# Kernel optimization log

Hardware: AMD Instinct MI355X
Metric: run time of the kernel (lower is better)

The kernel has to match this reference:

```python
import jax, jax.numpy as jnp
import numpy as np

EPS = 1e-8
THRESHOLD_FACTOR = 0.5


def setup_inputs() -> dict:
    key = jax.random.key(0)
    k1, k2, k3 = jax.random.split(key, 3)
    B, S, D_IN, D_OUT = 4, 4096, 2048, 2048
    x = jax.random.normal(k1, (B, S, D_IN), dtype=jnp.float32)
    # kaiming-uniform-like init for weight
    bound = 1.0 / np.sqrt(D_IN)
    weight = jax.random.uniform(k2, (D_OUT, D_IN), dtype=jnp.float32,
                                minval=-np.sqrt(3.0) * bound, maxval=np.sqrt(3.0) * bound)
    row_scale = jnp.ones((D_OUT, 1), dtype=jnp.float32)
    bias = jax.random.uniform(k3, (D_OUT,), dtype=jnp.float32, minval=-bound, maxval=bound)
    g = jnp.ones((D_IN,), dtype=jnp.float32)  # input RMSNorm affine weight
    return {"x": x, "weight": weight, "row_scale": row_scale, "bias": bias, "g": g}


def _rms_norm(v, axis):
    return v * jax.lax.rsqrt(jnp.mean(v * v, axis=axis, keepdims=True) + EPS)


def reference(x, weight, row_scale, bias, g):
    # input RMSNorm with affine scale
    xn = _rms_norm(x, -1) * g  # [B,S,Din]
    # row RMSNorm of weight
    w = _rms_norm(weight, 1)  # [Dout,Din]
    # abs-mean threshold ternary quantization
    abs_mean = jnp.mean(jnp.abs(w), axis=1, keepdims=True)  # [Dout,1]
    mask = (jnp.abs(w) > THRESHOLD_FACTOR * abs_mean).astype(w.dtype)
    w_q = jnp.sign(w) * mask  # ternary {-1,0,1}
    # scaled dequant: per-row abs_mean and learned row_scale
    w_eff = w_q * abs_mean * row_scale  # [Dout,Din]
    out = jnp.einsum('bsd,od->bso', xn, w_eff) + bias
    return out
```

## Files before the change

kernel.cpp:

```cpp
#include <hip/hip_runtime.h>
#include <stdint.h>

#define EPSF 1e-8f

using i32x4 = __attribute__((ext_vector_type(4))) int;

__device__ __forceinline__ float wave_sum(float v) {
#pragma unroll
  for (int off = 32; off > 0; off >>= 1) v += __shfl_down(v, off, 64);
  return v;
}
__device__ __forceinline__ float wave_max(float v) {
#pragma unroll
  for (int off = 32; off > 0; off >>= 1) v = fmaxf(v, __shfl_down(v, off, 64));
  return v;
}

__global__ __launch_bounds__(256) void wquant_kernel(
    const float* __restrict__ w, const float* __restrict__ row_scale,
    signed char* __restrict__ wq, float* __restrict__ scale, int K) {
  const int row = blockIdx.x;
  const int t = threadIdx.x;
  const float* wr = w + (size_t)row * K;
  float4 v0 = reinterpret_cast<const float4*>(wr)[2 * t];
  float4 v1 = reinterpret_cast<const float4*>(wr)[2 * t + 1];
  float f[8] = {v0.x, v0.y, v0.z, v0.w, v1.x, v1.y, v1.z, v1.w};
  float sa = 0.f, sq = 0.f;
#pragma unroll
  for (int i = 0; i < 8; ++i) { sa += fabsf(f[i]); sq += f[i] * f[i]; }
  sa = wave_sum(sa);
  sq = wave_sum(sq);
  __shared__ float smA[4], smQ[4];
  const int wid = t >> 6;
  if ((t & 63) == 0) { smA[wid] = sa; smQ[wid] = sq; }
  __syncthreads();
  const float sumabs = smA[0] + smA[1] + smA[2] + smA[3];
  const float sumsq  = smQ[0] + smQ[1] + smQ[2] + smQ[3];
  const float absmean = sumabs / (float)K;
  const float thr = 0.5f * absmean;
  union { signed char c[8]; uint2 u; } pk;
#pragma unroll
  for (int i = 0; i < 8; ++i)
    pk.c[i] = (fabsf(f[i]) > thr) ? (f[i] > 0.f ? (signed char)1 : (signed char)-1)
                                  : (signed char)0;
  reinterpret_cast<uint2*>(wq + (size_t)row * K)[t] = pk.u;
  if (t == 0)
    scale[row] = absmean * rsqrtf(sumsq / (float)K + EPSF) * row_scale[row];
}

__global__ __launch_bounds__(256) void xnorm_kernel(
    const float* __restrict__ x, const float* __restrict__ g,
    signed char* __restrict__ xq, float* __restrict__ sx, int K) {
  const int row = blockIdx.x;
  const int t = threadIdx.x;
  const float* xr = x + (size_t)row * K;
  float4 v0 = reinterpret_cast<const float4*>(xr)[2 * t];
  float4 v1 = reinterpret_cast<const float4*>(xr)[2 * t + 1];
  float f[8] = {v0.x, v0.y, v0.z, v0.w, v1.x, v1.y, v1.z, v1.w};
  float sq = 0.f;
#pragma unroll
  for (int i = 0; i < 8; ++i) sq += f[i] * f[i];
  sq = wave_sum(sq);
  __shared__ float smQ[4], smM[4];
  const int wid = t >> 6;
  if ((t & 63) == 0) smQ[wid] = sq;
  __syncthreads();
  const float sumsq = smQ[0] + smQ[1] + smQ[2] + smQ[3];
  const float rs = rsqrtf(sumsq / (float)K + EPSF);
  float4 g0 = reinterpret_cast<const float4*>(g)[2 * t];
  float4 g1 = reinterpret_cast<const float4*>(g)[2 * t + 1];
  float gg[8] = {g0.x, g0.y, g0.z, g0.w, g1.x, g1.y, g1.z, g1.w};
  float vv[8]; float am = 0.f;
#pragma unroll
  for (int i = 0; i < 8; ++i) {
    vv[i] = f[i] * rs * gg[i];
    am = fmaxf(am, fabsf(vv[i]));
  }
  am = wave_max(am);
  if ((t & 63) == 0) smM[wid] = am;
  __syncthreads();
  const float amax = fmaxf(fmaxf(smM[0], smM[1]), fmaxf(smM[2], smM[3]));
  const float inv = amax > 0.f ? 127.f / amax : 0.f;
  union { signed char c[8]; uint2 u; } pk;
#pragma unroll
  for (int i = 0; i < 8; ++i)
    pk.c[i] = (signed char)__float2int_rn(vv[i] * inv);
  reinterpret_cast<uint2*>(xq + (size_t)row * K)[t] = pk.u;
  if (t == 0) sx[row] = amax > 0.f ? amax / 127.f : 0.f;
}


#define BAR() do { __builtin_amdgcn_sched_barrier(0); \
                   asm volatile("" ::: "memory"); \
                   __builtin_amdgcn_s_barrier(); \
                   asm volatile("" ::: "memory"); \
                   __builtin_amdgcn_sched_barrier(0); } while (0)
#define VM(n) asm volatile("s_waitcnt vmcnt(" #n ")" ::: "memory")

__global__ __launch_bounds__(512, 2) void gemm_kernel(
    const signed char* __restrict__ A,
    const signed char* __restrict__ B,
    const float* __restrict__ scale, const float* __restrict__ bias,
    const float* __restrict__ sx,
    float* __restrict__ C, int M, int N, int K) {
  __shared__ signed char lds[2][2][2][16384];

  const int tid  = threadIdx.x;
  const int lane = tid & 63;
  const int wid  = tid >> 6;
  const int wm   = wid >> 2;
  const int wn   = wid & 3;
  const int fr   = lane & 15;
  const int kq   = lane >> 4;

  const int nwg = gridDim.x;
  const int cpx = nwg >> 3;
  const int swz = (blockIdx.x & 7) * cpx + (blockIdx.x >> 3);
  const int NBN = N >> 8;
  const int bn = swz % NBN;
  const int bm = swz / NBN;
  const int mBase = bm * 256, nBase = bn * 256;

  const size_t Kb = (size_t)K;

  const int sr = tid >> 3;
  const int gsrc = (tid & 7) ^ (sr & 7);
  const char* Abyte = (const char*)A + (size_t)(mBase + sr) * Kb + gsrc * 16;
  const char* Bbyte = (const char*)B +
      (size_t)(nBase + ((sr >> 5) * 64) + (sr & 31)) * Kb + gsrc * 16;

#define STAGE_A(bufi, h, t) do { \
    __builtin_amdgcn_global_load_lds( \
      (const __attribute__((address_space(1))) void*)(Abyte + (size_t)((h) * 64) * Kb + (size_t)(t) * 128), \
      (__attribute__((address_space(3))) void*)(&lds[bufi][0][h][tid * 16]), 16, 0, 0); \
    __builtin_amdgcn_global_load_lds( \
      (const __attribute__((address_space(1))) void*)(Abyte + (size_t)(128 + (h) * 64) * Kb + (size_t)(t) * 128), \
      (__attribute__((address_space(3))) void*)(&lds[bufi][0][h][8192 + tid * 16]), 16, 0, 0); \
  } while (0)

#define STAGE_B(bufi, h, t) do { \
    __builtin_amdgcn_global_load_lds( \
      (const __attribute__((address_space(1))) void*)(Bbyte + (size_t)((h) * 32) * Kb + (size_t)(t) * 128), \
      (__attribute__((address_space(3))) void*)(&lds[bufi][1][h][tid * 16]), 16, 0, 0); \
    __builtin_amdgcn_global_load_lds( \
      (const __attribute__((address_space(1))) void*)(Bbyte + (size_t)(128 + (h) * 32) * Kb + (size_t)(t) * 128), \
      (__attribute__((address_space(3))) void*)(&lds[bufi][1][h][8192 + tid * 16]), 16, 0, 0); \
  } while (0)

  const int slot0 = ((kq ^ (fr & 7)) << 4);
  const int aRowB = (wm * 64 + fr) * 128;
  const int bRowB = (wn * 32 + fr) * 128;

  i32x4 aF[4][2], bF[4][2];
  i32x4 acc[8][4];
#pragma unroll
  for (int m = 0; m < 8; ++m)
#pragma unroll
    for (int n = 0; n < 4; ++n) acc[m][n] = (i32x4){0, 0, 0, 0};

#define LDA(bufi, mg) do { \
    _Pragma("unroll") for (int mm = 0; mm < 4; ++mm) \
    _Pragma("unroll") for (int s = 0; s < 2; ++s) \
      aF[mm][s] = *(const i32x4*)&lds[bufi][0][mg][ \
          aRowB + mm * 2048 + (slot0 ^ (s << 6))]; \
  } while (0)

#define LDB(bufi, np) do { \
    _Pragma("unroll") for (int nn = 0; nn < 2; ++nn) \
    _Pragma("unroll") for (int s = 0; s < 2; ++s) \
      bF[(np) * 2 + nn][s] = *(const i32x4*)&lds[bufi][1][np][ \
          bRowB + nn * 2048 + (slot0 ^ (s << 6))]; \
  } while (0)

#define MFMA_Q(mg, np) do { \
    __builtin_amdgcn_s_setprio(1); \
    _Pragma("unroll") for (int mm = 0; mm < 4; ++mm) \
    _Pragma("unroll") for (int nn = 0; nn < 2; ++nn) { \
      i32x4 c = acc[(mg) * 4 + mm][(np) * 2 + nn]; \
      c = __builtin_amdgcn_mfma_i32_16x16x64_i8(aF[mm][0], bF[(np) * 2 + nn][0], c, 0, 0, 0); \
      c = __builtin_amdgcn_mfma_i32_16x16x64_i8(aF[mm][1], bF[(np) * 2 + nn][1], c, 0, 0, 0); \
      acc[(mg) * 4 + mm][(np) * 2 + nn] = c; \
    } \
    __builtin_amdgcn_s_setprio(0); } while (0)

  const int crowBase = mBase + wm * 128 + kq * 4;
  const int ccolBase = nBase + wn * 64 + fr;

#define STORE_Q(mg, np) do { \
    float sxq_[4][4]; \
    _Pragma("unroll") for (int mm = 0; mm < 4; ++mm) \
    _Pragma("unroll") for (int r = 0; r < 4; ++r) \
      sxq_[mm][r] = sx[crowBase + ((mg) * 4 + mm) * 16 + r]; \
    _Pragma("unroll") for (int nn = 0; nn < 2; ++nn) { \
      const int gc = ccolBase + ((np) * 2 + nn) * 16; \
      const float sc = scale[gc]; \
      const float bi = bias[gc]; \
      _Pragma("unroll") for (int mm = 0; mm < 4; ++mm) { \
        const int r0 = crowBase + ((mg) * 4 + mm) * 16; \
        _Pragma("unroll") for (int r = 0; r < 4; ++r) \
          C[(size_t)(r0 + r) * (size_t)N + (size_t)gc] = \
              (float)acc[(mg) * 4 + mm][(np) * 2 + nn][r] * (sxq_[mm][r] * sc) + bi; \
      } } } while (0)

  STAGE_A(0, 0, 0); STAGE_B(0, 0, 0);
  STAGE_A(0, 1, 0); STAGE_B(0, 1, 0);
  STAGE_A(1, 0, 1); STAGE_B(1, 0, 1);

  const int NT = K >> 7;
  for (int i = 0; i < (NT >> 1) - 1; ++i) {
    const int t1  = 2 * i + 1;
    const int tn0 = 2 * i + 2;
    const int tn1 = 2 * i + 3;
    VM(4); BAR();
    STAGE_A(1, 1, t1); STAGE_B(1, 1, t1);
    LDA(0, 0); LDB(0, 0); LDB(0, 1);
    MFMA_Q(0, 0); MFMA_Q(0, 1);
    BAR();
    STAGE_A(0, 0, tn0); STAGE_B(0, 0, tn0);
    LDA(0, 1);
    MFMA_Q(1, 0); MFMA_Q(1, 1);
    VM(4); BAR();
    STAGE_A(0, 1, tn0); STAGE_B(0, 1, tn0);
    LDA(1, 0); LDB(1, 0); LDB(1, 1);
    MFMA_Q(0, 0); MFMA_Q(0, 1);
    BAR();
    STAGE_A(1, 0, tn1); STAGE_B(1, 0, tn1);
    LDA(1, 1);
    MFMA_Q(1, 0); MFMA_Q(1, 1);
  }

  {
    const int tl = NT - 1;
    VM(4); BAR();
    STAGE_A(1, 1, tl); STAGE_B(1, 1, tl);
    LDA(0, 0); LDB(0, 0); LDB(0, 1);
    MFMA_Q(0, 0); MFMA_Q(0, 1);
    BAR();
    LDA(0, 1);
    MFMA_Q(1, 0); MFMA_Q(1, 1);
    VM(0); BAR();
    LDA(1, 0); LDB(1, 0); LDB(1, 1);
    MFMA_Q(0, 0); STORE_Q(0, 0);
    MFMA_Q(0, 1); STORE_Q(0, 1);
    BAR();
    LDA(1, 1);
    MFMA_Q(1, 0); STORE_Q(1, 0);
    MFMA_Q(1, 1); STORE_Q(1, 1);
  }
#undef STAGE_A
#undef STAGE_B
#undef LDA
#undef LDB
#undef MFMA_Q
#undef STORE_Q
}

extern "C" void kernel_launch(void* const* d_in, const int* in_sizes, int n_in,
                              void* d_out, int out_size, void* d_ws, size_t ws_size,
                              hipStream_t stream) {
  const float* x         = (const float*)d_in[0];
  const float* weight    = (const float*)d_in[1];
  const float* row_scale = (const float*)d_in[2];
  const float* bias      = (const float*)d_in[3];
  const float* g         = (const float*)d_in[4];
  float* out = (float*)d_out;

  const int Din  = in_sizes[4];
  const int Dout = in_sizes[3];
  const int Mrows = in_sizes[0] / Din;

  char* ws = (char*)d_ws;
  signed char* wq = (signed char*)ws;
  signed char* xq = (signed char*)(ws + (size_t)Dout * Din);
  float* scale = (float*)(ws + (size_t)Dout * Din + (size_t)Mrows * Din);
  float* sx = scale + Dout;

  wquant_kernel<<<Dout, 256, 0, stream>>>(weight, row_scale, wq, scale, Din);
  xnorm_kernel<<<Mrows, 256, 0, stream>>>(x, g, xq, sx, Din);
  const int grid = (Mrows / 256) * (Dout / 256);
  gemm_kernel<<<grid, 512, 0, stream>>>(xq, wq, scale, bias, sx, out,
                                        Mrows, Dout, Din);
}
```

Baseline: 116.4 us.

## Load B fragments directly from global to registers and merge prep kernels

The GEMM stops staging the weight (B) tile through LDS and instead loads each wave's B fragments straight from global memory into registers, double-buffered across two register banks. The A-only LDS buffer is halved and the schedule is rewritten with new vmcnt waits. The two quantization kernels are also merged into one launch to save a kernel launch. The risks are uncoalesced or redundant global B reads across waves, since the four waves sharing a column no longer share an LDS copy, and fragile hand-counted vmcnt values.

```diff
diff --git a/kernel.cpp b/kernel.cpp
--- a/kernel.cpp
+++ b/kernel.cpp
@@ -16,77 +16,76 @@
   return v;
 }
 
-__global__ __launch_bounds__(256) void wquant_kernel(
+__global__ __launch_bounds__(256) void prep_kernel(
+    const float* __restrict__ x, const float* __restrict__ g,
     const float* __restrict__ w, const float* __restrict__ row_scale,
-    signed char* __restrict__ wq, float* __restrict__ scale, int K) {
-  const int row = blockIdx.x;
+    signed char* __restrict__ xq, float* __restrict__ sx,
+    signed char* __restrict__ wq, float* __restrict__ scale,
+    int K, int Dout) {
+  __shared__ float smA[4], smQ[4], smM[4];
   const int t = threadIdx.x;
-  const float* wr = w + (size_t)row * K;
-  float4 v0 = reinterpret_cast<const float4*>(wr)[2 * t];
-  float4 v1 = reinterpret_cast<const float4*>(wr)[2 * t + 1];
-  float f[8] = {v0.x, v0.y, v0.z, v0.w, v1.x, v1.y, v1.z, v1.w};
-  float sa = 0.f, sq = 0.f;
-#pragma unroll
-  for (int i = 0; i < 8; ++i) { sa += fabsf(f[i]); sq += f[i] * f[i]; }
-  sa = wave_sum(sa);
-  sq = wave_sum(sq);
-  __shared__ float smA[4], smQ[4];
   const int wid = t >> 6;
-  if ((t & 63) == 0) { smA[wid] = sa; smQ[wid] = sq; }
-  __syncthreads();
-  const float sumabs = smA[0] + smA[1] + smA[2] + smA[3];
-  const float sumsq  = smQ[0] + smQ[1] + smQ[2] + smQ[3];
-  const float absmean = sumabs / (float)K;
-  const float thr = 0.5f * absmean;
-  union { signed char c[8]; uint2 u; } pk;
-#pragma unroll
-  for (int i = 0; i < 8; ++i)
-    pk.c[i] = (fabsf(f[i]) > thr) ? (f[i] > 0.f ? (signed char)1 : (signed char)-1)
-                                  : (signed char)0;
-  reinterpret_cast<uint2*>(wq + (size_t)row * K)[t] = pk.u;
-  if (t == 0)
-    scale[row] = absmean * rsqrtf(sumsq / (float)K + EPSF) * row_scale[row];
-}
-
-__global__ __launch_bounds__(256) void xnorm_kernel(
-    const float* __restrict__ x, const float* __restrict__ g,
-    signed char* __restrict__ xq, float* __restrict__ sx, int K) {
-  const int row = blockIdx.x;
-  const int t = threadIdx.x;
-  const float* xr = x + (size_t)row * K;
-  float4 v0 = reinterpret_cast<const float4*>(xr)[2 * t];
-  float4 v1 = reinterpret_cast<const float4*>(xr)[2 * t + 1];
-  float f[8] = {v0.x, v0.y, v0.z, v0.w, v1.x, v1.y, v1.z, v1.w};
-  float sq = 0.f;
-#pragma unroll
-  for (int i = 0; i < 8; ++i) sq += f[i] * f[i];
-  sq = wave_sum(sq);
-  __shared__ float smQ[4], smM[4];
-  const int wid = t >> 6;
-  if ((t & 63) == 0) smQ[wid] = sq;
-  __syncthreads();
-  const float sumsq = smQ[0] + smQ[1] + smQ[2] + smQ[3];
-  const float rs = rsqrtf(sumsq / (float)K + EPSF);
-  float4 g0 = reinterpret_cast<const float4*>(g)[2 * t];
-  float4 g1 = reinterpret_cast<const float4*>(g)[2 * t + 1];
-  float gg[8] = {g0.x, g0.y, g0.z, g0.w, g1.x, g1.y, g1.z, g1.w};
-  float vv[8]; float am = 0.f;
-#pragma unroll
-  for (int i = 0; i < 8; ++i) {
-    vv[i] = f[i] * rs * gg[i];
-    am = fmaxf(am, fabsf(vv[i]));
+  if ((int)blockIdx.x < Dout) {
+    const int row = blockIdx.x;
+    const float* wr = w + (size_t)row * K;
+    float4 v0 = reinterpret_cast<const float4*>(wr)[2 * t];
+    float4 v1 = reinterpret_cast<const float4*>(wr)[2 * t + 1];
+    float f[8] = {v0.x, v0.y, v0.z, v0.w, v1.x, v1.y, v1.z, v1.w};
+    float sa = 0.f, sq = 0.f;
+#pragma unroll
+    for (int i = 0; i < 8; ++i) { sa += fabsf(f[i]); sq += f[i] * f[i]; }
+    sa = wave_sum(sa);
+    sq = wave_sum(sq);
+    if ((t & 63) == 0) { smA[wid] = sa; smQ[wid] = sq; }
+    __syncthreads();
+    const float sumabs = smA[0] + smA[1] + smA[2] + smA[3];
+    const float sumsq  = smQ[0] + smQ[1] + smQ[2] + smQ[3];
+    const float absmean = sumabs / (float)K;
+    const float thr = 0.5f * absmean;
+    union { signed char c[8]; uint2 u; } pk;
+#pragma unroll
+    for (int i = 0; i < 8; ++i)
+      pk.c[i] = (fabsf(f[i]) > thr)
+                    ? (f[i] > 0.f ? (signed char)1 : (signed char)-1)
+                    : (signed char)0;
+    reinterpret_cast<uint2*>(wq + (size_t)row * K)[t] = pk.u;
+    if (t == 0)
+      scale[row] = absmean * rsqrtf(sumsq / (float)K + EPSF) * row_scale[row];
+  } else {
+    const int row = blockIdx.x - Dout;
+    const float* xr = x + (size_t)row * K;
+    float4 v0 = reinterpret_cast<const float4*>(xr)[2 * t];
+    float4 v1 = reinterpret_cast<const float4*>(xr)[2 * t + 1];
+    float f[8] = {v0.x, v0.y, v0.z, v0.w, v1.x, v1.y, v1.z, v1.w};
+    float sq = 0.f;
+#pragma unroll
+    for (int i = 0; i < 8; ++i) sq += f[i] * f[i];
+    sq = wave_sum(sq);
+    if ((t & 63) == 0) smQ[wid] = sq;
+    __syncthreads();
+    const float sumsq = smQ[0] + smQ[1] + smQ[2] + smQ[3];
+    const float rs = rsqrtf(sumsq / (float)K + EPSF);
+    float4 g0 = reinterpret_cast<const float4*>(g)[2 * t];
+    float4 g1 = reinterpret_cast<const float4*>(g)[2 * t + 1];
+    float gg[8] = {g0.x, g0.y, g0.z, g0.w, g1.x, g1.y, g1.z, g1.w};
+    float vv[8]; float am = 0.f;
+#pragma unroll
+    for (int i = 0; i < 8; ++i) {
+      vv[i] = f[i] * rs * gg[i];
+      am = fmaxf(am, fabsf(vv[i]));
+    }
+    am = wave_max(am);
+    if ((t & 63) == 0) smM[wid] = am;
+    __syncthreads();
+    const float amax = fmaxf(fmaxf(smM[0], smM[1]), fmaxf(smM[2], smM[3]));
+    const float inv = amax > 0.f ? 127.f / amax : 0.f;
+    union { signed char c[8]; uint2 u; } pk;
+#pragma unroll
+    for (int i = 0; i < 8; ++i)
+      pk.c[i] = (signed char)__float2int_rn(vv[i] * inv);
+    reinterpret_cast<uint2*>(xq + (size_t)row * K)[t] = pk.u;
+    if (t == 0) sx[row] = amax > 0.f ? amax / 127.f : 0.f;
   }
-  am = wave_max(am);
-  if ((t & 63) == 0) smM[wid] = am;
-  __syncthreads();
-  const float amax = fmaxf(fmaxf(smM[0], smM[1]), fmaxf(smM[2], smM[3]));
-  const float inv = amax > 0.f ? 127.f / amax : 0.f;
-  union { signed char c[8]; uint2 u; } pk;
-#pragma unroll
-  for (int i = 0; i < 8; ++i)
-    pk.c[i] = (signed char)__float2int_rn(vv[i] * inv);
-  reinterpret_cast<uint2*>(xq + (size_t)row * K)[t] = pk.u;
-  if (t == 0) sx[row] = amax > 0.f ? amax / 127.f : 0.f;
 }
 
 
@@ -103,7 +102,7 @@
     const float* __restrict__ scale, const float* __restrict__ bias,
     const float* __restrict__ sx,
     float* __restrict__ C, int M, int N, int K) {
-  __shared__ signed char lds[2][2][2][16384];
+  __shared__ signed char lds[2][2][16384];
 
   const int tid  = threadIdx.x;
   const int lane = tid & 63;
@@ -126,32 +125,26 @@
   const int sr = tid >> 3;
   const int gsrc = (tid & 7) ^ (sr & 7);
   const char* Abyte = (const char*)A + (size_t)(mBase + sr) * Kb + gsrc * 16;
-  const char* Bbyte = (const char*)B +
-      (size_t)(nBase + ((sr >> 5) * 64) + (sr & 31)) * Kb + gsrc * 16;
 
 #define STAGE_A(bufi, h, t) do { \
     __builtin_amdgcn_global_load_lds( \
       (const __attribute__((address_space(1))) void*)(Abyte + (size_t)((h) * 64) * Kb + (size_t)(t) * 128), \
-      (__attribute__((address_space(3))) void*)(&lds[bufi][0][h][tid * 16]), 16, 0, 0); \
+      (__attribute__((address_space(3))) void*)(&lds[bufi][h][tid * 16]), 16, 0, 0); \
     __builtin_amdgcn_global_load_lds( \
       (const __attribute__((address_space(1))) void*)(Abyte + (size_t)(128 + (h) * 64) * Kb + (size_t)(t) * 128), \
-      (__attribute__((address_space(3))) void*)(&lds[bufi][0][h][8192 + tid * 16]), 16, 0, 0); \
-  } while (0)
-
-#define STAGE_B(bufi, h, t) do { \
-    __builtin_amdgcn_global_load_lds( \
-      (const __attribute__((address_space(1))) void*)(Bbyte + (size_t)((h) * 32) * Kb + (size_t)(t) * 128), \
-      (__attribute__((address_space(3))) void*)(&lds[bufi][1][h][tid * 16]), 16, 0, 0); \
-    __builtin_amdgcn_global_load_lds( \
-      (const __attribute__((address_space(1))) void*)(Bbyte + (size_t)(128 + (h) * 32) * Kb + (size_t)(t) * 128), \
-      (__attribute__((address_space(3))) void*)(&lds[bufi][1][h][8192 + tid * 16]), 16, 0, 0); \
+      (__attribute__((address_space(3))) void*)(&lds[bufi][h][8192 + tid * 16]), 16, 0, 0); \
   } while (0)
 
   const int slot0 = ((kq ^ (fr & 7)) << 4);
   const int aRowB = (wm * 64 + fr) * 128;
-  const int bRowB = (wn * 32 + fr) * 128;
-
-  i32x4 aF[4][2], bF[4][2];
+
+  const uint32_t bo0 = (uint32_t)((nBase + wn * 64 + fr) * K) + kq * 16;
+  const uint32_t bo1 = bo0 + (uint32_t)(16 * K);
+  const uint32_t bo2 = bo0 + (uint32_t)(32 * K);
+  const uint32_t bo3 = bo0 + (uint32_t)(48 * K);
+
+  i32x4 aF[4][2];
+  i32x4 bN0[2][2], bN1[2][2];
   i32x4 acc[8][4];
 #pragma unroll
   for (int m = 0; m < 8; ++m)
@@ -161,24 +154,33 @@
 #define LDA(bufi, mg) do { \
     _Pragma("unroll") for (int mm = 0; mm < 4; ++mm) \
     _Pragma("unroll") for (int s = 0; s < 2; ++s) \
-      aF[mm][s] = *(const i32x4*)&lds[bufi][0][mg][ \
+      aF[mm][s] = *(const i32x4*)&lds[bufi][mg][ \
           aRowB + mm * 2048 + (slot0 ^ (s << 6))]; \
   } while (0)
 
-#define LDB(bufi, np) do { \
-    _Pragma("unroll") for (int nn = 0; nn < 2; ++nn) \
-    _Pragma("unroll") for (int s = 0; s < 2; ++s) \
-      bF[(np) * 2 + nn][s] = *(const i32x4*)&lds[bufi][1][np][ \
-          bRowB + nn * 2048 + (slot0 ^ (s << 6))]; \
-  } while (0)
-
-#define MFMA_Q(mg, np) do { \
+#define LBN0(kt) do { \
+    const signed char* Bk_ = B + (size_t)(kt) * 128; \
+    bN0[0][0] = *(const i32x4*)(Bk_ + bo0); \
+    bN0[0][1] = *(const i32x4*)(Bk_ + bo0 + 64); \
+    bN0[1][0] = *(const i32x4*)(Bk_ + bo1); \
+    bN0[1][1] = *(const i32x4*)(Bk_ + bo1 + 64); \
+  } while (0)
+
+#define LBN1(kt) do { \
+    const signed char* Bk_ = B + (size_t)(kt) * 128; \
+    bN1[0][0] = *(const i32x4*)(Bk_ + bo2); \
+    bN1[0][1] = *(const i32x4*)(Bk_ + bo2 + 64); \
+    bN1[1][0] = *(const i32x4*)(Bk_ + bo3); \
+    bN1[1][1] = *(const i32x4*)(Bk_ + bo3 + 64); \
+  } while (0)
+
+#define MFMA_Q(mg, np, bank) do { \
     __builtin_amdgcn_s_setprio(1); \
     _Pragma("unroll") for (int mm = 0; mm < 4; ++mm) \
     _Pragma("unroll") for (int nn = 0; nn < 2; ++nn) { \
       i32x4 c = acc[(mg) * 4 + mm][(np) * 2 + nn]; \
-      c = __builtin_amdgcn_mfma_i32_16x16x64_i8(aF[mm][0], bF[(np) * 2 + nn][0], c, 0, 0, 0); \
-      c = __builtin_amdgcn_mfma_i32_16x16x64_i8(aF[mm][1], bF[(np) * 2 + nn][1], c, 0, 0, 0); \
+      c = __builtin_amdgcn_mfma_i32_16x16x64_i8(aF[mm][0], bank[nn][0], c, 0, 0, 0); \
+      c = __builtin_amdgcn_mfma_i32_16x16x64_i8(aF[mm][1], bank[nn][1], c, 0, 0, 0); \
       acc[(mg) * 4 + mm][(np) * 2 + nn] = c; \
     } \
     __builtin_amdgcn_s_setprio(0); } while (0)
@@ -202,55 +204,58 @@
               (float)acc[(mg) * 4 + mm][(np) * 2 + nn][r] * (sxq_[mm][r] * sc) + bi; \
       } } } while (0)
 
-  STAGE_A(0, 0, 0); STAGE_B(0, 0, 0);
-  STAGE_A(0, 1, 0); STAGE_B(0, 1, 0);
-  STAGE_A(1, 0, 1); STAGE_B(1, 0, 1);
+  STAGE_A(0, 0, 0);
+  STAGE_A(0, 1, 0);
+  STAGE_A(1, 0, 1);
+  __builtin_amdgcn_sched_barrier(0);
+  LBN0(0);
+  VM(4);
+  BAR();
 
   const int NT = K >> 7;
   for (int i = 0; i < (NT >> 1) - 1; ++i) {
+    const int t0  = 2 * i;
     const int t1  = 2 * i + 1;
     const int tn0 = 2 * i + 2;
     const int tn1 = 2 * i + 3;
-    VM(4); BAR();
-    STAGE_A(1, 1, t1); STAGE_B(1, 1, t1);
-    LDA(0, 0); LDB(0, 0); LDB(0, 1);
-    MFMA_Q(0, 0); MFMA_Q(0, 1);
-    BAR();
-    STAGE_A(0, 0, tn0); STAGE_B(0, 0, tn0);
-    LDA(0, 1);
-    MFMA_Q(1, 0); MFMA_Q(1, 1);
-    VM(4); BAR();
-    STAGE_A(0, 1, tn0); STAGE_B(0, 1, tn0);
-    LDA(1, 0); LDB(1, 0); LDB(1, 1);
-    MFMA_Q(0, 0); MFMA_Q(0, 1);
-    BAR();
-    STAGE_A(1, 0, tn1); STAGE_B(1, 0, tn1);
-    LDA(1, 1);
-    MFMA_Q(1, 0); MFMA_Q(1, 1);
+    VM(16); LDA(0, 0); STAGE_A(1, 1, t1); LBN1(t0);
+    BAR(); MFMA_Q(0, 0, bN0);
+    BAR(); MFMA_Q(0, 1, bN1);
+    VM(12); LDA(0, 1); STAGE_A(0, 0, tn0);
+    BAR(); MFMA_Q(1, 0, bN0);
+    LBN0(t1);
+    BAR(); MFMA_Q(1, 1, bN1);
+    VM(16); LDA(1, 0); STAGE_A(0, 1, tn0); LBN1(t1);
+    BAR(); MFMA_Q(0, 0, bN0);
+    BAR(); MFMA_Q(0, 1, bN1);
+    VM(12); LDA(1, 1); STAGE_A(1, 0, tn1);
+    BAR(); MFMA_Q(1, 0, bN0);
+    LBN0(tn0);
+    BAR(); MFMA_Q(1, 1, bN1);
   }
 
   {
+    const int tp = NT - 2;
     const int tl = NT - 1;
-    VM(4); BAR();
-    STAGE_A(1, 1, tl); STAGE_B(1, 1, tl);
-    LDA(0, 0); LDB(0, 0); LDB(0, 1);
-    MFMA_Q(0, 0); MFMA_Q(0, 1);
-    BAR();
-    LDA(0, 1);
-    MFMA_Q(1, 0); MFMA_Q(1, 1);
-    VM(0); BAR();
-    LDA(1, 0); LDB(1, 0); LDB(1, 1);
-    MFMA_Q(0, 0); STORE_Q(0, 0);
-    MFMA_Q(0, 1); STORE_Q(0, 1);
-    BAR();
-    LDA(1, 1);
-    MFMA_Q(1, 0); STORE_Q(1, 0);
-    MFMA_Q(1, 1); STORE_Q(1, 1);
+    VM(16); LDA(0, 0); STAGE_A(1, 1, tl); LBN1(tp);
+    BAR(); MFMA_Q(0, 0, bN0);
+    BAR(); MFMA_Q(0, 1, bN1);
+    VM(12); LDA(0, 1);
+    BAR(); MFMA_Q(1, 0, bN0);
+    LBN0(tl);
+    BAR(); MFMA_Q(1, 1, bN1);
+    VM(12); LDA(1, 0); LBN1(tl);
+    BAR(); MFMA_Q(0, 0, bN0); STORE_Q(0, 0);
+    BAR(); MFMA_Q(0, 1, bN1); STORE_Q(0, 1);
+    VM(8); LDA(1, 1);
+    BAR(); MFMA_Q(1, 0, bN0); STORE_Q(1, 0);
+    BAR(); MFMA_Q(1, 1, bN1); STORE_Q(1, 1);
   }
+  VM(0);
 #undef STAGE_A
-#undef STAGE_B
 #undef LDA
-#undef LDB
+#undef LBN0
+#undef LBN1
 #undef MFMA_Q
 #undef STORE_Q
 }
@@ -275,8 +280,8 @@
   float* scale = (float*)(ws + (size_t)Dout * Din + (size_t)Mrows * Din);
   float* sx = scale + Dout;
 
-  wquant_kernel<<<Dout, 256, 0, stream>>>(weight, row_scale, wq, scale, Din);
-  xnorm_kernel<<<Mrows, 256, 0, stream>>>(x, g, xq, sx, Din);
+  prep_kernel<<<Dout + Mrows, 256, 0, stream>>>(x, g, weight, row_scale,
+                                                xq, sx, wq, scale, Din, Dout);
   const int grid = (Mrows / 256) * (Dout / 256);
   gemm_kernel<<<grid, 512, 0, stream>>>(xq, wq, scale, bias, sx, out,
                                         Mrows, Dout, Din);
```

After: 146.9 us. 1.26x slower.
